# Kernel tuning notes

Measured on AMD Instinct MI355X. Metric: run time of the kernel, lower is better.

Reference implementation:

```python
import jax, jax.numpy as jnp
import numpy as np

KSIZE = 7
HEAD_DIM = 64
EPS = 1e-6

def rmsnorm(x, w):
    return x * jax.lax.rsqrt(jnp.mean(x * x, axis=-1, keepdims=True) + EPS) * w

def rope2d(x):
    # Split channels: first half rotated by row position, second half by column position.
    B, H, W, C = x.shape
    half = C // 2
    q = half // 2
    inv = 1.0 / (10000.0 ** (jnp.arange(q, dtype=jnp.float32) / q))
    th_y = jnp.arange(H, dtype=jnp.float32)[:, None] * inv  # [H,q]
    th_x = jnp.arange(W, dtype=jnp.float32)[:, None] * inv  # [W,q]
    def rot(v, th):  # v: [...,q,2], th broadcastable to [...,q]
        c, s = jnp.cos(th), jnp.sin(th)
        a, b = v[..., 0], v[..., 1]
        return jnp.stack([a * c - b * s, a * s + b * c], axis=-1)
    xy = rot(x[..., :half].reshape(B, H, W, q, 2), th_y[None, :, None, :])
    xx = rot(x[..., half:].reshape(B, H, W, q, 2), th_x[None, None, :, :])
    return jnp.concatenate([xy.reshape(B, H, W, half), xx.reshape(B, H, W, half)], axis=-1)

def neighborhood_attn(x, w_qkv, w_proj, b_proj, k=KSIZE, hd=HEAD_DIM):
    # NATTEN semantics: each query attends to a k x k window; window start is
    # clamped at borders so every query sees exactly k*k keys.
    B, H, W, C = x.shape
    nh = C // hd
    qkv = x @ w_qkv                           # [B,H,W,3C]
    qv, kv, vv = jnp.split(qkv, 3, axis=-1)
    qh = qv.reshape(B, H, W, nh, hd)
    kh = kv.reshape(B, H, W, nh, hd)
    vh = vv.reshape(B, H, W, nh, hd)
    idx_h = jnp.clip(jnp.arange(H) - k // 2, 0, H - k)[:, None] + jnp.arange(k)  # [H,k]
    idx_w = jnp.clip(jnp.arange(W) - k // 2, 0, W - k)[:, None] + jnp.arange(k)  # [W,k]
    def gather(t):  # [B,H,W,nh,hd] -> [B,H,W,nh,k*k,hd]
        g = t[:, idx_h]            # [B,H,k,W,nh,hd]
        g = g[:, :, :, idx_w]      # [B,H,k,W,k,nh,hd]
        return g.transpose(0, 1, 3, 5, 2, 4, 6).reshape(B, H, W, nh, k * k, hd)
    kn = gather(kh)
    vn = gather(vh)
    scale = 1.0 / np.sqrt(hd).astype(np.float32)
    logits = jnp.einsum('bxynd,bxynkd->bxynk', qh, kn) * scale
    attn = jax.nn.softmax(logits, axis=-1)
    out = jnp.einsum('bxynk,bxynkd->bxynd', attn, vn).reshape(B, H, W, C)
    return out @ w_proj + b_proj

def geglu(x, ff1_w, ff1_b, ff2_w, ff2_b):
    h = x @ ff1_w + ff1_b
    gate, value = jnp.split(h, 2, axis=-1)
    return (jax.nn.gelu(gate, approximate=False) * value) @ ff2_w + ff2_b

def setup_inputs():
    key = jax.random.key(0)
    B, H, W, C = 2, 64, 64, 256
    ks = jax.random.split(key, 8)
    g = lambda k, shape, sc: jax.random.normal(k, shape, jnp.float32) * sc
    return {
        'x': g(ks[0], (B, H, W, C), 1.0),
        'norm1_w': jnp.ones((C,), jnp.float32),
        'norm2_w': jnp.ones((C,), jnp.float32),
        'w_qkv': g(ks[1], (C, 3 * C), 0.02),
        'w_proj': g(ks[2], (C, C), 0.02),
        'b_proj': g(ks[3], (C,), 0.02),
        'ff1_w': g(ks[4], (C, 2 * C), 0.02),
        'ff1_b': g(ks[5], (2 * C,), 0.02),
        'ff2_w': g(ks[6], (C, C), 0.02),
        'ff2_b': g(ks[7], (C,), 0.02),
    }

def reference(x, norm1_w, norm2_w, w_qkv, w_proj, b_proj, ff1_w, ff1_b, ff2_w, ff2_b):
    h = rope2d(rmsnorm(x, norm1_w))
    x = x + neighborhood_attn(h, w_qkv, w_proj, b_proj)
    x = x + geglu(rmsnorm(x, norm2_w), ff1_w, ff1_b, ff2_w, ff2_b)
    return x
```

## Files before the change

### kernel.cpp

```cpp
#include <hip/hip_runtime.h>
#include <hip/hip_bf16.h>


#define ROWS 8192
typedef unsigned int uint32;
typedef unsigned short ushort16;
typedef __attribute__((ext_vector_type(8))) short short8;
typedef __attribute__((ext_vector_type(4))) float floatx4;

__device__ __forceinline__ float bf2f(__hip_bfloat16 b) { return __bfloat162float(b); }
__device__ __forceinline__ float us2f(ushort16 u) {
    return __uint_as_float(((uint32)u) << 16);
}
__device__ __forceinline__ ushort16 f2us(float f) {
    __hip_bfloat16 h = __float2bfloat16(f);
    return *(ushort16*)&h;
}
__device__ __forceinline__ float ldflag(const void* p, size_t i, int f32) {
    return f32 ? ((const float*)p)[i] : bf2f(((const __hip_bfloat16*)p)[i]);
}

__device__ __forceinline__ void gl_lds16(const void* gptr, void* lptr) {
    __builtin_amdgcn_global_load_lds(
        (const __attribute__((address_space(1))) uint32*)gptr,
        (__attribute__((address_space(3))) uint32*)lptr, 16, 0, 0);
}

__global__ __launch_bounds__(64) void detect_kernel(const ushort16* __restrict__ xu,
                                                    int* __restrict__ flag) {
    const int lane = threadIdx.x;
    const float v = us2f(xu[lane * 62]);
    const float a = fabsf(v);
    const bool sane = (a < 1e4f) && (a > 1e-8f);
    const unsigned long long m = __ballot(sane);
    if (lane == 0) flag[0] = (__popcll(m) < 32) ? 1 : 0;
}

struct WSrc {
    const void *wqkv, *wproj, *ff1w, *ff2w, *bproj, *ff1b, *ff2b;
};
__global__ __launch_bounds__(256) void cvt_kernel(WSrc s, ushort16* __restrict__ wT,
                                                  float* __restrict__ bF,
                                                  const int* __restrict__ flag) {
    const int f32 = flag[0];
    const int bid = blockIdx.x, tid = threadIdx.x;
    if (bid == 112) {
        #pragma unroll
        for (int it = 0; it < 4; ++it) {
            const int j = it * 256 + tid;
            float v;
            if (j < 256)      v = ldflag(s.bproj, j, f32);
            else if (j < 768) v = ldflag(s.ff1b, j - 256, f32);
            else              v = ldflag(s.ff2b, j - 768, f32);
            bF[j] = v;
        }
        return;
    }
    const void* src; int N, kt, nt, base;
    if (bid < 48)      { src = s.wqkv;  N = 768; kt = bid / 12;      nt = bid % 12;      base = 0; }
    else if (bid < 64) { const int l = bid - 48; src = s.wproj; N = 256; kt = l / 4; nt = l % 4; base = 196608; }
    else if (bid < 96) { const int l = bid - 64; src = s.ff1w;  N = 512; kt = l / 8; nt = l % 8; base = 262144; }
    else               { const int l = bid - 96; src = s.ff2w;  N = 256; kt = l / 4; nt = l % 4; base = 393216; }

    __shared__ ushort16 T[64][65];
    const int r0 = tid >> 6, c = tid & 63;
    #pragma unroll
    for (int j = 0; j < 16; ++j) {
        const int r = j * 4 + r0;
        T[r][c] = f2us(ldflag(src, (size_t)(kt * 64 + r) * N + nt * 64 + c, f32));
    }
    __syncthreads();
    const int n = tid >> 2, kg = tid & 3;
    #pragma unroll
    for (int j = 0; j < 16; ++j) {
        const int k = kg * 16 + j;
        wT[base + (size_t)(nt * 64 + n) * 256 + kt * 64 + k] = T[k][n];
    }
}

__global__ __launch_bounds__(256) void fused_qkv(const void* __restrict__ x,
                                                 const void* __restrict__ n1w,
                                                 const ushort16* __restrict__ wqkvT,
                                                 ushort16* __restrict__ qkv,
                                                 const int* __restrict__ flag) {
    __shared__ ushort16 Apad[32 * 264];
    __shared__ ushort16 Bs[256 * 32];

    const int f32 = flag[0];
    const int tid = threadIdx.x, lane = tid & 63, wid = tid >> 6;
    const int l15 = lane & 15, kq8 = (lane >> 4) * 8;
    const int n0 = blockIdx.x * 256, m0 = blockIdx.y * 32;
    const int nw = wid * 64;
    const int cr = lane >> 2, cc = (lane & 3) * 8;

    {
        const int row = tid >> 3, s = tid & 7;
        const int gm = m0 + row;
        float v[32];
        #pragma unroll
        for (int j = 0; j < 8; ++j) {
            const size_t off = (size_t)gm * 256 + s * 32 + j * 4;
            if (f32) {
                const float4 d = *(const float4*)((const float*)x + off);
                v[j * 4] = d.x; v[j * 4 + 1] = d.y; v[j * 4 + 2] = d.z; v[j * 4 + 3] = d.w;
            } else {
                const ushort4 d = *(const ushort4*)((const ushort16*)x + off);
                v[j * 4] = us2f(d.x); v[j * 4 + 1] = us2f(d.y);
                v[j * 4 + 2] = us2f(d.z); v[j * 4 + 3] = us2f(d.w);
            }
        }
        float sq = 0.0f;
        #pragma unroll
        for (int i = 0; i < 32; ++i) sq += v[i] * v[i];
        sq += __shfl_xor(sq, 1);
        sq += __shfl_xor(sq, 2);
        sq += __shfl_xor(sq, 4);
        const float rr = rsqrtf(sq * (1.0f / 256.0f) + 1e-6f);

        const int py = (gm >> 6) & 63, px = gm & 63;
        #pragma unroll
        for (int j = 0; j < 8; ++j) {
            const int c0 = s * 32 + j * 4;
            float nv[4];
            #pragma unroll
            for (int u = 0; u < 4; ++u)
                nv[u] = v[j * 4 + u] * rr * ldflag(n1w, c0 + u, f32);
            const float pos = (c0 < 128) ? (float)py : (float)px;
            const int j0 = (c0 & 127) >> 1;
            #pragma unroll
            for (int p = 0; p < 2; ++p) {
                const float inv = expf(-(float)(j0 + p) * (9.210340371976184f / 64.0f));
                const float th = pos * inv;
                const float cs = cosf(th), sn = sinf(th);
                const float a = nv[p * 2], b = nv[p * 2 + 1];
                nv[p * 2]     = a * cs - b * sn;
                nv[p * 2 + 1] = a * sn + b * cs;
            }
            ushort4 o;
            o.x = f2us(nv[0]); o.y = f2us(nv[1]); o.z = f2us(nv[2]); o.w = f2us(nv[3]);
            *(ushort4*)&Apad[row * 264 + c0] = o;
        }
    }
    __syncthreads();

    floatx4 acc[2][4] = {};
    for (int k0 = 0; k0 < 256; k0 += 32) {
        #pragma unroll
        for (int c = 0; c < 4; ++c) {
            const int ch = wid + c * 4;
            gl_lds16(wqkvT + (size_t)(n0 + ch * 16 + cr) * 256 + k0 + cc, Bs + ch * 512);
        }
        __syncthreads();
        short8 af[2], bf[4];
        #pragma unroll
        for (int mi = 0; mi < 2; ++mi)
            af[mi] = *(const short8*)&Apad[(mi * 16 + l15) * 264 + k0 + kq8];
        #pragma unroll
        for (int nj = 0; nj < 4; ++nj)
            bf[nj] = *(const short8*)&Bs[(nw + nj * 16 + l15) * 32 + kq8];
        #pragma unroll
        for (int mi = 0; mi < 2; ++mi)
            #pragma unroll
            for (int nj = 0; nj < 4; ++nj)
                acc[mi][nj] = __builtin_amdgcn_mfma_f32_16x16x32_bf16(af[mi], bf[nj], acc[mi][nj], 0, 0, 0);
        __syncthreads();
    }

    const int crow = (lane >> 4) * 4;
    #pragma unroll
    for (int mi = 0; mi < 2; ++mi)
        #pragma unroll
        for (int nj = 0; nj < 4; ++nj)
            #pragma unroll
            for (int r = 0; r < 4; ++r) {
                const int m = m0 + mi * 16 + crow + r;
                const int n = n0 + nw + nj * 16 + l15;
                qkv[(size_t)m * 768 + n] = f2us(acc[mi][nj][r]);
            }
}

__global__ __launch_bounds__(256) void attn_kernel(const ushort16* __restrict__ qkv,
                                                   ushort16* __restrict__ ao) {
    __shared__ ushort16 smem[40208];
    ushort16* const KS = smem;
    ushort16* const VT = smem + 12544;
    ushort16* const PL = smem + 26880;

    const int tid = threadIdx.x, lane = tid & 63, wid = tid >> 6;
    const int l15 = lane & 15, kq8 = (lane >> 4) * 8;
    const int bid = blockIdx.x;
    const int h = bid & 3;
    const int t = (bid >> 2) & 63;
    const int b = bid >> 8;
    const int ty0 = (t >> 3) * 8, tx0 = (t & 7) * 8;
    const int hby = min(max(ty0 - 3, 0), 50);
    const int hbx = min(max(tx0 - 3, 0), 50);
    const int hcol = h * 64;

    const int qpl = wid * 16 + l15;
    const int qpy = ty0 + (qpl >> 3), qpx = tx0 + (qpl & 7);
    const size_t qoff = (size_t)(b * 4096 + qpy * 64 + qpx) * 768 + hcol + kq8;
    const short8 af0 = *(const short8*)&qkv[qoff];
    const short8 af1 = *(const short8*)&qkv[qoff + 32];

    for (int it = tid; it < 3136; it += 256) {
        const bool isK = it < 1568;
        const int task = isK ? it : it - 1568;
        const int key = task >> 3, oct = task & 7;
        const int pix = b * 4096 + (hby + key / 14) * 64 + hbx + key % 14;
        const uint4 d = *(const uint4*)&qkv[(size_t)pix * 768 + (isK ? 256 : 512) + hcol + oct * 8];
        if (isK) {
            uint32* dst = (uint32*)&KS[(oct >> 2) * 6272 + key * 32 + (oct & 3) * 8];
            dst[0] = d.x; dst[1] = d.y; dst[2] = d.z; dst[3] = d.w;
        } else {
            const ushort16* s8 = (const ushort16*)&d;
            #pragma unroll
            for (int j = 0; j < 8; ++j) VT[(oct * 8 + j) * 224 + key] = s8[j];
        }
    }
    for (int it = tid; it < 1792; it += 256)
        VT[(it / 28) * 224 + 196 + (it % 28)] = 0;
    __syncthreads();

    floatx4 acc[13];
    #pragma unroll
    for (int nt = 0; nt < 13; ++nt) {
        const int krow = (nt * 16 + l15) * 32 + kq8;
        const short8 bf0 = *(const short8*)&KS[krow];
        const short8 bf1 = *(const short8*)&KS[6272 + krow];
        floatx4 a = {0.0f, 0.0f, 0.0f, 0.0f};
        a = __builtin_amdgcn_mfma_f32_16x16x32_bf16(af0, bf0, a, 0, 0, 0);
        a = __builtin_amdgcn_mfma_f32_16x16x32_bf16(af1, bf1, a, 0, 0, 0);
        acc[nt] = a;
    }

    int kyA[13], kxA[13];
    #pragma unroll
    for (int nt = 0; nt < 13; ++nt) {
        const int kidx = nt * 16 + l15;
        kyA[nt] = hby + kidx / 14;
        kxA[nt] = hbx + kidx % 14;
    }

    const int crow = (lane >> 4) * 4;
    float rs[4];
    #pragma unroll
    for (int r = 0; r < 4; ++r) {
        const int pl = wid * 16 + crow + r;
        const int py = ty0 + (pl >> 3), px = tx0 + (pl & 7);
        const int sy = min(max(py - 3, 0), 57), sx = min(max(px - 3, 0), 57);
        float lv[13];
        float mx = -1e30f;
        #pragma unroll
        for (int nt = 0; nt < 13; ++nt) {
            const int kidx = nt * 16 + l15;
            const bool valid = (kidx < 196) &&
                               ((unsigned)(kyA[nt] - sy) < 7u) &&
                               ((unsigned)(kxA[nt] - sx) < 7u);
            lv[nt] = valid ? acc[nt][r] * 0.125f : -1e30f;
            mx = fmaxf(mx, lv[nt]);
        }
        #pragma unroll
        for (int off = 1; off < 16; off <<= 1) mx = fmaxf(mx, __shfl_xor(mx, off));
        float sme = 0.0f;
        #pragma unroll
        for (int nt = 0; nt < 13; ++nt) {
            const float e = exp2f((lv[nt] - mx) * 1.4426950408889634f);
            lv[nt] = e;
            sme += e;
        }
        #pragma unroll
        for (int off = 1; off < 16; off <<= 1) sme += __shfl_xor(sme, off);
        rs[r] = 1.0f / sme;
        #pragma unroll
        for (int nt = 0; nt < 13; ++nt)
            PL[pl * 208 + nt * 16 + l15] = f2us(lv[nt]);
    }
    __syncthreads();

    floatx4 oacc[4] = {};
    #pragma unroll
    for (int kc = 0; kc < 7; ++kc) {
        const short8 af = *(const short8*)&PL[(wid * 16 + l15) * 208 + kc * 32 + kq8];
        #pragma unroll
        for (int nd = 0; nd < 4; ++nd) {
            const short8 bf = *(const short8*)&VT[(nd * 16 + l15) * 224 + kc * 32 + kq8];
            oacc[nd] = __builtin_amdgcn_mfma_f32_16x16x32_bf16(af, bf, oacc[nd], 0, 0, 0);
        }
    }
    #pragma unroll
    for (int r = 0; r < 4; ++r) {
        const int pl = wid * 16 + crow + r;
        const int py = ty0 + (pl >> 3), px = tx0 + (pl & 7);
        const size_t o = (size_t)(b * 4096 + py * 64 + px) * 256 + hcol;
        #pragma unroll
        for (int nd = 0; nd < 4; ++nd)
            ao[o + nd * 16 + l15] = f2us(oacc[nd][r] * rs[r]);
    }
}

__global__ __launch_bounds__(256) void gemm_proj_rms(const ushort16* __restrict__ A,
                                                     const ushort16* __restrict__ Bt,
                                                     const float* __restrict__ bias,
                                                     const void* __restrict__ xres,
                                                     const void* __restrict__ n2w,
                                                     float* __restrict__ x1,
                                                     ushort16* __restrict__ y,
                                                     const int* __restrict__ flag) {
    constexpr int TM = 2, TN = 4;
    __shared__ ushort16 At[32 * 32];
    __shared__ ushort16 Bs[256 * 32];
    __shared__ float red[4][32];

    const int f32 = flag[0];
    const int tid = threadIdx.x, lane = tid & 63, wid = tid >> 6;
    const int m0 = blockIdx.x * 32;
    const int nw = wid * 64;
    const int cr = lane >> 2, cc = (lane & 3) * 8;
    const int l15 = lane & 15, kq = (lane >> 4) * 8;

    floatx4 acc[TM][TN] = {};

    for (int k0 = 0; k0 < 256; k0 += 32) {
        #pragma unroll
        for (int c = 0; c < 5; ++c) {
            const int ch = wid + c * 4;
            if (ch < 18) {
                const ushort16* g;
                ushort16* l;
                if (ch < 2) {
                    g = A + (size_t)(m0 + ch * 16 + cr) * 256 + k0 + cc;
                    l = At + ch * 512;
                } else {
                    const int c2 = ch - 2;
                    g = Bt + (size_t)(c2 * 16 + cr) * 256 + k0 + cc;
                    l = Bs + c2 * 512;
                }
                gl_lds16(g, l);
            }
        }
        __syncthreads();

        short8 af[TM], bf[TN];
        #pragma unroll
        for (int mi = 0; mi < TM; ++mi)
            af[mi] = *(const short8*)&At[(mi * 16 + l15) * 32 + kq];
        #pragma unroll
        for (int nj = 0; nj < TN; ++nj)
            bf[nj] = *(const short8*)&Bs[(nw + nj * 16 + l15) * 32 + kq];
        #pragma unroll
        for (int mi = 0; mi < TM; ++mi)
            #pragma unroll
            for (int nj = 0; nj < TN; ++nj)
                acc[mi][nj] = __builtin_amdgcn_mfma_f32_16x16x32_bf16(af[mi], bf[nj], acc[mi][nj], 0, 0, 0);
        __syncthreads();
    }

    const int crow = (lane >> 4) * 4;
    float w2[TN], bsv[TN];
    #pragma unroll
    for (int nj = 0; nj < TN; ++nj) {
        const int n = nw + nj * 16 + l15;
        w2[nj] = ldflag(n2w, n, f32);
        bsv[nj] = bias[n];
    }

    float ps[TM][4] = {};
    #pragma unroll
    for (int mi = 0; mi < TM; ++mi)
        #pragma unroll
        for (int nj = 0; nj < TN; ++nj)
            #pragma unroll
            for (int r = 0; r < 4; ++r) {
                const int m = m0 + mi * 16 + crow + r;
                const int n = nw + nj * 16 + l15;
                float v = acc[mi][nj][r] + bsv[nj] + ldflag(xres, (size_t)m * 256 + n, f32);
                acc[mi][nj][r] = v;
                ps[mi][r] += v * v;
            }
    #pragma unroll
    for (int off = 1; off < 16; off <<= 1)
        #pragma unroll
        for (int mi = 0; mi < TM; ++mi)
            #pragma unroll
            for (int r = 0; r < 4; ++r) ps[mi][r] += __shfl_xor(ps[mi][r], off);
    if (l15 == 0)
        #pragma unroll
        for (int mi = 0; mi < TM; ++mi)
            #pragma unroll
            for (int r = 0; r < 4; ++r) red[wid][mi * 16 + crow + r] = ps[mi][r];
    __syncthreads();

    float rr[TM][4];
    #pragma unroll
    for (int mi = 0; mi < TM; ++mi)
        #pragma unroll
        for (int r = 0; r < 4; ++r) {
            const int row = mi * 16 + crow + r;
            const float s = red[0][row] + red[1][row] + red[2][row] + red[3][row];
            rr[mi][r] = rsqrtf(s * (1.0f / 256.0f) + 1e-6f);
        }
    #pragma unroll
    for (int mi = 0; mi < TM; ++mi)
        #pragma unroll
        for (int nj = 0; nj < TN; ++nj)
            #pragma unroll
            for (int r = 0; r < 4; ++r) {
                const int m = m0 + mi * 16 + crow + r;
                const int n = nw + nj * 16 + l15;
                const size_t oi = (size_t)m * 256 + n;
                const float v = acc[mi][nj][r];
                x1[oi] = v;
                y[oi] = f2us(v * rr[mi][r] * w2[nj]);
            }
}

__global__ __launch_bounds__(256) void fused_ffn(const ushort16* __restrict__ y,
                                                 const ushort16* __restrict__ ff1wT,
                                                 const ushort16* __restrict__ ff2wT,
                                                 const float* __restrict__ bF,
                                                 const float* __restrict__ x1,
                                                 void* __restrict__ out,
                                                 const int* __restrict__ flag) {
    __shared__ ushort16 Apad[32 * 264];
    __shared__ ushort16 Bs[512 * 32];

    const int f32 = flag[0];
    const int tid = threadIdx.x, lane = tid & 63, wid = tid >> 6;
    const int l15 = lane & 15, kq8 = (lane >> 4) * 8;
    const int m0 = blockIdx.x * 32;
    const int cr = lane >> 2, cc = (lane & 3) * 8;
    const int crow = (lane >> 4) * 4;

    {
        const int row = tid >> 3, s = tid & 7;
        #pragma unroll
        for (int j = 0; j < 4; ++j) {
            const int c = s * 32 + j * 8;
            const uint4 d = *(const uint4*)&y[(size_t)(m0 + row) * 256 + c];
            *(uint4*)&Apad[row * 264 + c] = d;
        }
    }
    __syncthreads();

    floatx4 accg[2][4] = {}, accv[2][4] = {};
    for (int k0 = 0; k0 < 256; k0 += 32) {
        #pragma unroll
        for (int c = 0; c < 8; ++c) {
            const int ch = wid + c * 4;
            gl_lds16(ff1wT + (size_t)(ch * 16 + cr) * 256 + k0 + cc, Bs + ch * 512);
        }
        __syncthreads();
        short8 af[2], bg[4], bv[4];
        #pragma unroll
        for (int mi = 0; mi < 2; ++mi)
            af[mi] = *(const short8*)&Apad[(mi * 16 + l15) * 264 + k0 + kq8];
        #pragma unroll
        for (int nj = 0; nj < 4; ++nj) {
            bg[nj] = *(const short8*)&Bs[(wid * 64 + nj * 16 + l15) * 32 + kq8];
            bv[nj] = *(const short8*)&Bs[(256 + wid * 64 + nj * 16 + l15) * 32 + kq8];
        }
        #pragma unroll
        for (int mi = 0; mi < 2; ++mi)
            #pragma unroll
            for (int nj = 0; nj < 4; ++nj) {
                accg[mi][nj] = __builtin_amdgcn_mfma_f32_16x16x32_bf16(af[mi], bg[nj], accg[mi][nj], 0, 0, 0);
                accv[mi][nj] = __builtin_amdgcn_mfma_f32_16x16x32_bf16(af[mi], bv[nj], accv[mi][nj], 0, 0, 0);
            }
        __syncthreads();
    }

    #pragma unroll
    for (int mi = 0; mi < 2; ++mi)
        #pragma unroll
        for (int nj = 0; nj < 4; ++nj) {
            const int n = wid * 64 + nj * 16 + l15;
            const float bg_ = bF[256 + n], bv_ = bF[512 + n];
            #pragma unroll
            for (int r = 0; r < 4; ++r) {
                const float gate = accg[mi][nj][r] + bg_;
                const float val = accv[mi][nj][r] + bv_;
                const float ge = 0.5f * gate * (1.0f + erff(gate * 0.70710678118654752f));
                Apad[(mi * 16 + crow + r) * 264 + n] = f2us(ge * val);
            }
        }
    __syncthreads();

    floatx4 acc2[2][4] = {};
    for (int k0 = 0; k0 < 256; k0 += 32) {
        #pragma unroll
        for (int c = 0; c < 4; ++c) {
            const int ch = wid + c * 4;
            gl_lds16(ff2wT + (size_t)(ch * 16 + cr) * 256 + k0 + cc, Bs + ch * 512);
        }
        __syncthreads();
        short8 af[2], bf[4];
        #pragma unroll
        for (int mi = 0; mi < 2; ++mi)
            af[mi] = *(const short8*)&Apad[(mi * 16 + l15) * 264 + k0 + kq8];
        #pragma unroll
        for (int nj = 0; nj < 4; ++nj)
            bf[nj] = *(const short8*)&Bs[(wid * 64 + nj * 16 + l15) * 32 + kq8];
        #pragma unroll
        for (int mi = 0; mi < 2; ++mi)
            #pragma unroll
            for (int nj = 0; nj < 4; ++nj)
                acc2[mi][nj] = __builtin_amdgcn_mfma_f32_16x16x32_bf16(af[mi], bf[nj], acc2[mi][nj], 0, 0, 0);
        __syncthreads();
    }

    #pragma unroll
    for (int mi = 0; mi < 2; ++mi)
        #pragma unroll
        for (int nj = 0; nj < 4; ++nj) {
            const int n = wid * 64 + nj * 16 + l15;
            const float bs = bF[768 + n];
            #pragma unroll
            for (int r = 0; r < 4; ++r) {
                const int m = m0 + mi * 16 + crow + r;
                const size_t oi = (size_t)m * 256 + n;
                const float v = acc2[mi][nj][r] + bs + x1[oi];
                if (f32) ((float*)out)[oi] = v;
                else     ((ushort16*)out)[oi] = f2us(v);
            }
        }
}

extern "C" void kernel_launch(void* const* d_in, const int* in_sizes, int n_in,
                              void* d_out, int out_size, void* d_ws, size_t ws_size,
                              hipStream_t stream) {
    const void* x   = d_in[0];
    const void* n1w = d_in[1];
    const void* n2w = d_in[2];
    WSrc ws_src{d_in[3], d_in[4], d_in[6], d_in[8], d_in[5], d_in[7], d_in[9]};

    char* ws = (char*)d_ws;
    int*      flag = (int*)ws;
    ushort16* wT   = (ushort16*)(ws + 4096);
    float*    bF   = (float*)(ws + 4096 + 458752 * 2);
    ushort16* y    = (ushort16*)(ws + (1 << 20));
    ushort16* qkv  = (ushort16*)(ws + (5 << 20));
    ushort16* ao   = (ushort16*)(ws + (size_t)(17 << 20));
    float*    x1   = (float*)(ws + (size_t)(21 << 20));

    ushort16* wqkvT  = wT;
    ushort16* wprojT = wT + 196608;
    ushort16* ff1wT  = wT + 262144;
    ushort16* ff2wT  = wT + 393216;

    detect_kernel<<<1, 64, 0, stream>>>((const ushort16*)x, flag);
    cvt_kernel<<<113, 256, 0, stream>>>(ws_src, wT, bF, flag);
    fused_qkv<<<dim3(3, 256), 256, 0, stream>>>(x, n1w, wqkvT, qkv, flag);
    attn_kernel<<<512, 256, 0, stream>>>(qkv, ao);
    gemm_proj_rms<<<256, 256, 0, stream>>>(ao, wprojT, bF, x, n2w, x1, y, flag);
    fused_ffn<<<256, 256, 0, stream>>>(y, ff1wT, ff2wT, bF, x1, d_out, flag);
}
```

Measured before the change: 156.2 us.

## Fuse projection, RMSNorm and GEGLU FFN into one tail kernel; add RoPE LUT

Merges the attention-projection/RMSNorm kernel with the FFN kernel so the residual x1 and the normalized y stay in registers and LDS instead of going through global memory. The RoPE cos/sin values are precomputed into a lookup table by an extra block of the weight-conversion kernel, replacing per-element expf/cosf/sinf. Exact erff in GELU is replaced by the Abramowitz-Stegun polynomial approximation, which has small error (~1e-7 abs). The fused kernel uses more LDS per block, which may lower occupancy.

Result: faster. 147.7 us, median of 2 (-5.5%).

```diff
diff --git a/kernel.cpp b/kernel.cpp
--- a/kernel.cpp
+++ b/kernel.cpp
@@ -24,6 +24,17 @@
     __builtin_amdgcn_global_load_lds(
         (const __attribute__((address_space(1))) uint32*)gptr,
         (__attribute__((address_space(3))) uint32*)lptr, 16, 0, 0);
+}
+
+__device__ __forceinline__ float gelu_f(float gate) {
+    const float z = gate * 0.70710678118654752f;
+    const float az = fabsf(z);
+    const float t1 = 1.0f / fmaf(0.3275911f, az, 1.0f);
+    const float poly = ((((1.061405429f * t1 - 1.453152027f) * t1 + 1.421413741f) * t1
+                         - 0.284496736f) * t1 + 0.254829592f) * t1;
+    float erfv = 1.0f - poly * __expf(-az * az);
+    erfv = (z < 0.0f) ? -erfv : erfv;
+    return 0.5f * gate * (1.0f + erfv);
 }
 
 __global__ __launch_bounds__(64) void detect_kernel(const ushort16* __restrict__ xu,
@@ -41,6 +52,7 @@
 };
 __global__ __launch_bounds__(256) void cvt_kernel(WSrc s, ushort16* __restrict__ wT,
                                                   float* __restrict__ bF,
+                                                  float2* __restrict__ lut,
                                                   const int* __restrict__ flag) {
     const int f32 = flag[0];
     const int bid = blockIdx.x, tid = threadIdx.x;
@@ -56,6 +68,17 @@
         }
         return;
     }
+    if (bid == 113) {
+        #pragma unroll
+        for (int it = 0; it < 16; ++it) {
+            const int idx = it * 256 + tid;
+            const int pos = idx >> 6, j = idx & 63;
+            const float inv = expf(-(float)j * (9.210340371976184f / 64.0f));
+            const float th = (float)pos * inv;
+            lut[idx] = make_float2(cosf(th), sinf(th));
+        }
+        return;
+    }
     const void* src; int N, kt, nt, base;
     if (bid < 48)      { src = s.wqkv;  N = 768; kt = bid / 12;      nt = bid % 12;      base = 0; }
     else if (bid < 64) { const int l = bid - 48; src = s.wproj; N = 256; kt = l / 4; nt = l % 4; base = 196608; }
@@ -81,6 +104,7 @@
 __global__ __launch_bounds__(256) void fused_qkv(const void* __restrict__ x,
                                                  const void* __restrict__ n1w,
                                                  const ushort16* __restrict__ wqkvT,
+                                                 const float2* __restrict__ lut,
                                                  ushort16* __restrict__ qkv,
                                                  const int* __restrict__ flag) {
     __shared__ ushort16 Apad[32 * 264];
@@ -125,16 +149,14 @@
             #pragma unroll
             for (int u = 0; u < 4; ++u)
                 nv[u] = v[j * 4 + u] * rr * ldflag(n1w, c0 + u, f32);
-            const float pos = (c0 < 128) ? (float)py : (float)px;
+            const int pos = (c0 < 128) ? py : px;
             const int j0 = (c0 & 127) >> 1;
             #pragma unroll
             for (int p = 0; p < 2; ++p) {
-                const float inv = expf(-(float)(j0 + p) * (9.210340371976184f / 64.0f));
-                const float th = pos * inv;
-                const float cs = cosf(th), sn = sinf(th);
+                const float2 cs = lut[pos * 64 + j0 + p];
                 const float a = nv[p * 2], b = nv[p * 2 + 1];
-                nv[p * 2]     = a * cs - b * sn;
-                nv[p * 2 + 1] = a * sn + b * cs;
+                nv[p * 2]     = a * cs.x - b * cs.y;
+                nv[p * 2 + 1] = a * cs.y + b * cs.x;
             }
             ushort4 o;
             o.x = f2us(nv[0]); o.y = f2us(nv[1]); o.z = f2us(nv[2]); o.w = f2us(nv[3]);
@@ -299,17 +321,18 @@
     }
 }
 
-__global__ __launch_bounds__(256) void gemm_proj_rms(const ushort16* __restrict__ A,
-                                                     const ushort16* __restrict__ Bt,
-                                                     const float* __restrict__ bias,
-                                                     const void* __restrict__ xres,
-                                                     const void* __restrict__ n2w,
-                                                     float* __restrict__ x1,
-                                                     ushort16* __restrict__ y,
-                                                     const int* __restrict__ flag) {
-    constexpr int TM = 2, TN = 4;
+__global__ __launch_bounds__(256) void fused_tail(const ushort16* __restrict__ A,
+                                                  const ushort16* __restrict__ wprojT,
+                                                  const ushort16* __restrict__ ff1wT,
+                                                  const ushort16* __restrict__ ff2wT,
+                                                  const float* __restrict__ bF,
+                                                  const void* __restrict__ xres,
+                                                  const void* __restrict__ n2w,
+                                                  void* __restrict__ out,
+                                                  const int* __restrict__ flag) {
     __shared__ ushort16 At[32 * 32];
-    __shared__ ushort16 Bs[256 * 32];
+    __shared__ ushort16 Apad[32 * 264];
+    __shared__ ushort16 Bs[512 * 32];
     __shared__ float red[4][32];
 
     const int f32 = flag[0];
@@ -318,9 +341,9 @@
     const int nw = wid * 64;
     const int cr = lane >> 2, cc = (lane & 3) * 8;
     const int l15 = lane & 15, kq = (lane >> 4) * 8;
-
-    floatx4 acc[TM][TN] = {};
-
+    const int crow = (lane >> 4) * 4;
+
+    floatx4 acc[2][4] = {};
     for (int k0 = 0; k0 < 256; k0 += 32) {
         #pragma unroll
         for (int c = 0; c < 5; ++c) {
@@ -333,43 +356,40 @@
                     l = At + ch * 512;
                 } else {
                     const int c2 = ch - 2;
-                    g = Bt + (size_t)(c2 * 16 + cr) * 256 + k0 + cc;
+                    g = wprojT + (size_t)(c2 * 16 + cr) * 256 + k0 + cc;
                     l = Bs + c2 * 512;
                 }
                 gl_lds16(g, l);
             }
         }
         __syncthreads();
-
-        short8 af[TM], bf[TN];
-        #pragma unroll
-        for (int mi = 0; mi < TM; ++mi)
+        short8 af[2], bf[4];
+        #pragma unroll
+        for (int mi = 0; mi < 2; ++mi)
             af[mi] = *(const short8*)&At[(mi * 16 + l15) * 32 + kq];
         #pragma unroll
-        for (int nj = 0; nj < TN; ++nj)
+        for (int nj = 0; nj < 4; ++nj)
             bf[nj] = *(const short8*)&Bs[(nw + nj * 16 + l15) * 32 + kq];
         #pragma unroll
-        for (int mi = 0; mi < TM; ++mi)
-            #pragma unroll
-            for (int nj = 0; nj < TN; ++nj)
+        for (int mi = 0; mi < 2; ++mi)
+            #pragma unroll
+            for (int nj = 0; nj < 4; ++nj)
                 acc[mi][nj] = __builtin_amdgcn_mfma_f32_16x16x32_bf16(af[mi], bf[nj], acc[mi][nj], 0, 0, 0);
         __syncthreads();
     }
 
-    const int crow = (lane >> 4) * 4;
-    float w2[TN], bsv[TN];
-    #pragma unroll
-    for (int nj = 0; nj < TN; ++nj) {
+    float w2[4], bsv[4];
+    #pragma unroll
+    for (int nj = 0; nj < 4; ++nj) {
         const int n = nw + nj * 16 + l15;
         w2[nj] = ldflag(n2w, n, f32);
-        bsv[nj] = bias[n];
-    }
-
-    float ps[TM][4] = {};
-    #pragma unroll
-    for (int mi = 0; mi < TM; ++mi)
-        #pragma unroll
-        for (int nj = 0; nj < TN; ++nj)
+        bsv[nj] = bF[n];
+    }
+    float ps[2][4] = {};
+    #pragma unroll
+    for (int mi = 0; mi < 2; ++mi)
+        #pragma unroll
+        for (int nj = 0; nj < 4; ++nj)
             #pragma unroll
             for (int r = 0; r < 4; ++r) {
                 const int m = m0 + mi * 16 + crow + r;
@@ -381,67 +401,28 @@
     #pragma unroll
     for (int off = 1; off < 16; off <<= 1)
         #pragma unroll
-        for (int mi = 0; mi < TM; ++mi)
+        for (int mi = 0; mi < 2; ++mi)
             #pragma unroll
             for (int r = 0; r < 4; ++r) ps[mi][r] += __shfl_xor(ps[mi][r], off);
     if (l15 == 0)
         #pragma unroll
-        for (int mi = 0; mi < TM; ++mi)
+        for (int mi = 0; mi < 2; ++mi)
             #pragma unroll
             for (int r = 0; r < 4; ++r) red[wid][mi * 16 + crow + r] = ps[mi][r];
     __syncthreads();
-
-    float rr[TM][4];
-    #pragma unroll
-    for (int mi = 0; mi < TM; ++mi)
+    #pragma unroll
+    for (int mi = 0; mi < 2; ++mi)
         #pragma unroll
         for (int r = 0; r < 4; ++r) {
             const int row = mi * 16 + crow + r;
             const float s = red[0][row] + red[1][row] + red[2][row] + red[3][row];
-            rr[mi][r] = rsqrtf(s * (1.0f / 256.0f) + 1e-6f);
-        }
-    #pragma unroll
-    for (int mi = 0; mi < TM; ++mi)
-        #pragma unroll
-        for (int nj = 0; nj < TN; ++nj)
-            #pragma unroll
-            for (int r = 0; r < 4; ++r) {
-                const int m = m0 + mi * 16 + crow + r;
+            const float rr = rsqrtf(s * (1.0f / 256.0f) + 1e-6f);
+            #pragma unroll
+            for (int nj = 0; nj < 4; ++nj) {
                 const int n = nw + nj * 16 + l15;
-                const size_t oi = (size_t)m * 256 + n;
-                const float v = acc[mi][nj][r];
-                x1[oi] = v;
-                y[oi] = f2us(v * rr[mi][r] * w2[nj]);
-            }
-}
-
-__global__ __launch_bounds__(256) void fused_ffn(const ushort16* __restrict__ y,
-                                                 const ushort16* __restrict__ ff1wT,
-                                                 const ushort16* __restrict__ ff2wT,
-                                                 const float* __restrict__ bF,
-                                                 const float* __restrict__ x1,
-                                                 void* __restrict__ out,
-                                                 const int* __restrict__ flag) {
-    __shared__ ushort16 Apad[32 * 264];
-    __shared__ ushort16 Bs[512 * 32];
-
-    const int f32 = flag[0];
-    const int tid = threadIdx.x, lane = tid & 63, wid = tid >> 6;
-    const int l15 = lane & 15, kq8 = (lane >> 4) * 8;
-    const int m0 = blockIdx.x * 32;
-    const int cr = lane >> 2, cc = (lane & 3) * 8;
-    const int crow = (lane >> 4) * 4;
-
-    {
-        const int row = tid >> 3, s = tid & 7;
-        #pragma unroll
-        for (int j = 0; j < 4; ++j) {
-            const int c = s * 32 + j * 8;
-            const uint4 d = *(const uint4*)&y[(size_t)(m0 + row) * 256 + c];
-            *(uint4*)&Apad[row * 264 + c] = d;
-        }
-    }
-    __syncthreads();
+                Apad[row * 264 + n] = f2us(acc[mi][nj][r] * rr * w2[nj]);
+            }
+        }
 
     floatx4 accg[2][4] = {}, accv[2][4] = {};
     for (int k0 = 0; k0 < 256; k0 += 32) {
@@ -454,11 +435,11 @@
         short8 af[2], bg[4], bv[4];
         #pragma unroll
         for (int mi = 0; mi < 2; ++mi)
-            af[mi] = *(const short8*)&Apad[(mi * 16 + l15) * 264 + k0 + kq8];
+            af[mi] = *(const short8*)&Apad[(mi * 16 + l15) * 264 + k0 + kq];
         #pragma unroll
         for (int nj = 0; nj < 4; ++nj) {
-            bg[nj] = *(const short8*)&Bs[(wid * 64 + nj * 16 + l15) * 32 + kq8];
-            bv[nj] = *(const short8*)&Bs[(256 + wid * 64 + nj * 16 + l15) * 32 + kq8];
+            bg[nj] = *(const short8*)&Bs[(nw + nj * 16 + l15) * 32 + kq];
+            bv[nj] = *(const short8*)&Bs[(256 + nw + nj * 16 + l15) * 32 + kq];
         }
         #pragma unroll
         for (int mi = 0; mi < 2; ++mi)
@@ -474,14 +455,13 @@
     for (int mi = 0; mi < 2; ++mi)
         #pragma unroll
         for (int nj = 0; nj < 4; ++nj) {
-            const int n = wid * 64 + nj * 16 + l15;
+            const int n = nw + nj * 16 + l15;
             const float bg_ = bF[256 + n], bv_ = bF[512 + n];
             #pragma unroll
             for (int r = 0; r < 4; ++r) {
                 const float gate = accg[mi][nj][r] + bg_;
                 const float val = accv[mi][nj][r] + bv_;
-                const float ge = 0.5f * gate * (1.0f + erff(gate * 0.70710678118654752f));
-                Apad[(mi * 16 + crow + r) * 264 + n] = f2us(ge * val);
+                Apad[(mi * 16 + crow + r) * 264 + n] = f2us(gelu_f(gate) * val);
             }
         }
     __syncthreads();
@@ -497,10 +477,10 @@
         short8 af[2], bf[4];
         #pragma unroll
         for (int mi = 0; mi < 2; ++mi)
-            af[mi] = *(const short8*)&Apad[(mi * 16 + l15) * 264 + k0 + kq8];
+            af[mi] = *(const short8*)&Apad[(mi * 16 + l15) * 264 + k0 + kq];
         #pragma unroll
         for (int nj = 0; nj < 4; ++nj)
-            bf[nj] = *(const short8*)&Bs[(wid * 64 + nj * 16 + l15) * 32 + kq8];
+            bf[nj] = *(const short8*)&Bs[(nw + nj * 16 + l15) * 32 + kq];
         #pragma unroll
         for (int mi = 0; mi < 2; ++mi)
             #pragma unroll
@@ -513,13 +493,13 @@
     for (int mi = 0; mi < 2; ++mi)
         #pragma unroll
         for (int nj = 0; nj < 4; ++nj) {
-            const int n = wid * 64 + nj * 16 + l15;
+            const int n = nw + nj * 16 + l15;
             const float bs = bF[768 + n];
             #pragma unroll
             for (int r = 0; r < 4; ++r) {
                 const int m = m0 + mi * 16 + crow + r;
                 const size_t oi = (size_t)m * 256 + n;
-                const float v = acc2[mi][nj][r] + bs + x1[oi];
+                const float v = acc2[mi][nj][r] + bs + acc[mi][nj][r];
                 if (f32) ((float*)out)[oi] = v;
                 else     ((ushort16*)out)[oi] = f2us(v);
             }
@@ -537,11 +517,10 @@
     char* ws = (char*)d_ws;
     int*      flag = (int*)ws;
     ushort16* wT   = (ushort16*)(ws + 4096);
-    float*    bF   = (float*)(ws + 4096 + 458752 * 2);
-    ushort16* y    = (ushort16*)(ws + (1 << 20));
+    float*    bF   = (float*)(ws + 921600);
+    float2*   lut  = (float2*)(ws + 925696);
     ushort16* qkv  = (ushort16*)(ws + (5 << 20));
     ushort16* ao   = (ushort16*)(ws + (size_t)(17 << 20));
-    float*    x1   = (float*)(ws + (size_t)(21 << 20));
 
     ushort16* wqkvT  = wT;
     ushort16* wprojT = wT + 196608;
@@ -549,9 +528,8 @@
     ushort16* ff2wT  = wT + 393216;
 
     detect_kernel<<<1, 64, 0, stream>>>((const ushort16*)x, flag);
-    cvt_kernel<<<113, 256, 0, stream>>>(ws_src, wT, bF, flag);
-    fused_qkv<<<dim3(3, 256), 256, 0, stream>>>(x, n1w, wqkvT, qkv, flag);
+    cvt_kernel<<<114, 256, 0, stream>>>(ws_src, wT, bF, lut, flag);
+    fused_qkv<<<dim3(3, 256), 256, 0, stream>>>(x, n1w, wqkvT, lut, qkv, flag);
     attn_kernel<<<512, 256, 0, stream>>>(qkv, ao);
-    gemm_proj_rms<<<256, 256, 0, stream>>>(ao, wprojT, bF, x, n2w, x1, y, flag);
-    fused_ffn<<<256, 256, 0, stream>>>(y, ff1wT, ff2wT, bF, x1, d_out, flag);
-}
+    fused_tail<<<256, 256, 0, stream>>>(ao, wprojT, ff1wT, ff2wT, bF, x, n2w, d_out, flag);
+}
```
